# Optimization experiments

Hardware: AMD Instinct MI355X
Metric: run time of the kernel (lower is better)

The kernel has to match this reference:

```python
import jax, jax.numpy as jnp
import numpy as np

MODEL_BATCHES = 2048
NUM_POINTS = 8192
N_FUNCS = 8
REMOVE_ITERS = 51  # remove_points = 51 * model_batches -> first 51 iterations dropped


def setup_inputs() -> dict:
    key = jax.random.key(0)
    k1, k2, k3, k4, k5 = jax.random.split(key, 5)
    point = jax.random.normal(k1, (MODEL_BATCHES, 2, 1), dtype=jnp.float32) * 0.1
    optimized_weights = jax.random.normal(k2, (N_FUNCS, 2, 2), dtype=jnp.float32) * 0.5
    optimized_biases = jax.random.normal(k3, (N_FUNCS, 2, 1), dtype=jnp.float32) * 0.5
    optimized_function_ops = jax.random.uniform(k4, (N_FUNCS,), dtype=jnp.float32)
    index = jax.random.randint(k5, (MODEL_BATCHES, NUM_POINTS), 0, N_FUNCS, dtype=jnp.int32)
    return {
        "point": point,
        "optimized_weights": optimized_weights,
        "optimized_biases": optimized_biases,
        "optimized_function_ops": optimized_function_ops,
        "index": index,
    }


def reference(point, optimized_weights, optimized_biases, optimized_function_ops, index):
    mb = point.shape[0]

    def step(p, idx):  # p: [mb,2,1], idx: [mb]
        W = optimized_weights[idx]          # [mb,2,2]
        b = optimized_biases[idx]           # [mb,2,1]
        op = optimized_function_ops[idx]    # [mb]
        p_new = jnp.einsum('bij,bjk->bik', W, p) + b  # [mb,2,1]
        out = jnp.concatenate([p_new[:, :, 0], op[:, None]], axis=1)  # [mb,3]
        return p_new, out

    # scan over iterations: index.T is [num_points, mb]
    _, outs = jax.lax.scan(step, point, index.T)  # outs: [num_points, mb, 3]
    pts = outs.reshape(-1, 3)  # matches torch.cat along dim 0 then squeeze
    return pts[REMOVE_ITERS * mb:, :]
```

## Files before the change

kernel.cpp:

```cpp
#include <hip/hip_runtime.h>
#include <hip/hip_fp16.h>

#define MB   2048
#define NP   8192
#define NF   8
#define RM   51
#define NCH  128
#define CH   64
#define NW   16

typedef float        f32x4 __attribute__((ext_vector_type(4)));
typedef unsigned int u32;


__device__ __forceinline__ void build_tbl(u32 (*tbl)[4], const float* W,
                                          const float* B, const float* OPS, int tid)
{
    if (tid < NF) {
        const __half2 h0 = __floats2half2_rn(W[tid*4+0], W[tid*4+1]);
        const __half2 h1 = __floats2half2_rn(W[tid*4+2], W[tid*4+3]);
        const __half2 h2 = __floats2half2_rn(B[tid*2+0], B[tid*2+1]);
        const __half2 h3 = __floats2half2_rn(OPS ? OPS[tid] : 0.f, 0.f);
        tbl[tid][0] = __builtin_bit_cast(u32, h0);
        tbl[tid][1] = __builtin_bit_cast(u32, h1);
        tbl[tid][2] = __builtin_bit_cast(u32, h2);
        tbl[tid][3] = __builtin_bit_cast(u32, h3);
    }
}

__global__ __launch_bounds__(256, 4) void ifs_phase1(
    const int* __restrict__ idxg, const float* __restrict__ W,
    const float* __restrict__ B,
    float4* __restrict__ mapsA, float2* __restrict__ mapsC, u32* __restrict__ codes)
{
    __shared__ u32 ptile[256][NW + 1];
    __shared__ __align__(16) u32 tbl[NF][4];
    const int tid = threadIdx.x;
    build_tbl(tbl, W, B, nullptr, tid);

    const int c  = blockIdx.x >> 3;
    const int b0 = (blockIdx.x & 7) << 8;
    const int x8 = tid & 7, yy = tid >> 3;

    auto stage = [&](int seg) {
        #pragma unroll
        for (int p = 0; p < 8; ++p) {
            const int row = yy + p * 32;
            const int4 v = *(const int4*)(idxg + (size_t)(b0 + row) * NP
                                          + c * CH + seg * 32 + x8 * 4);
            ptile[row][seg * 8 + x8] =
                (u32)v.x | ((u32)v.y << 8) | ((u32)v.z << 16) | ((u32)v.w << 24);
        }
    };
    stage(0);
    __syncthreads();

    float a00 = 1.f, a01 = 0.f, a10 = 0.f, a11 = 1.f, c0 = 0.f, c1 = 0.f;
    for (int seg = 0; seg < 2; ++seg) {
        if (seg == 0) stage(1);
        #pragma unroll
        for (int j = 0; j < 8; ++j) {
            const u32 pc = ptile[tid][seg * 8 + j];
            #pragma unroll
            for (int e = 0; e < 4; ++e) {
                const int f = (pc >> (8 * e)) & 7;
                const uint4 u = *(const uint4*)&tbl[f][0];
                const float2 w0 = __half22float2(__builtin_bit_cast(__half2, u.x));
                const float2 w1 = __half22float2(__builtin_bit_cast(__half2, u.y));
                const float2 bb = __half22float2(__builtin_bit_cast(__half2, u.z));
                const float na00 = w0.x*a00 + w0.y*a10;
                const float na01 = w0.x*a01 + w0.y*a11;
                const float na10 = w1.x*a00 + w1.y*a10;
                const float na11 = w1.x*a01 + w1.y*a11;
                const float nc0  = w0.x*c0  + w0.y*c1 + bb.x;
                const float nc1  = w1.x*c0  + w1.y*c1 + bb.y;
                a00 = na00; a01 = na01; a10 = na10; a11 = na11; c0 = nc0; c1 = nc1;
            }
        }
        __syncthreads();
    }
    #pragma unroll
    for (int w = 0; w < NW; ++w)
        codes[((size_t)c * NW + w) * MB + b0 + tid] = ptile[tid][w];
    mapsA[(size_t)c * MB + b0 + tid] = make_float4(a00, a01, a10, a11);
    mapsC[(size_t)c * MB + b0 + tid] = make_float2(c0, c1);
}

__global__ __launch_bounds__(64) void ifs_phase2(
    const float2* __restrict__ point, const float4* __restrict__ mapsA,
    const float2* __restrict__ mapsC, float2* __restrict__ pe)
{
    const int b = blockIdx.x * 64 + threadIdx.x;
    float2 p = point[b];
    float4 A0[8], A1[8]; float2 C0[8], C1[8];
    #pragma unroll
    for (int k = 0; k < 8; ++k) {
        A0[k] = mapsA[(size_t)k * MB + b];
        C0[k] = mapsC[(size_t)k * MB + b];
    }
    for (int g = 0; g < 16; ++g) {
        if (g < 15) {
            #pragma unroll
            for (int k = 0; k < 8; ++k) {
                A1[k] = mapsA[(size_t)((g + 1) * 8 + k) * MB + b];
                C1[k] = mapsC[(size_t)((g + 1) * 8 + k) * MB + b];
            }
        }
        #pragma unroll
        for (int k = 0; k < 8; ++k) {
            pe[(size_t)(g * 8 + k) * MB + b] = p;
            const float nx = A0[k].x * p.x + A0[k].y * p.y + C0[k].x;
            const float ny = A0[k].z * p.x + A0[k].w * p.y + C0[k].y;
            p.x = nx; p.y = ny;
        }
        #pragma unroll
        for (int k = 0; k < 8; ++k) { A0[k] = A1[k]; C0[k] = C1[k]; }
    }
}

__global__ __launch_bounds__(256, 4) void ifs_phase3(
    const u32* __restrict__ codes, const float* __restrict__ W,
    const float* __restrict__ B, const float* __restrict__ OPS,
    const float2* __restrict__ pe, float* __restrict__ out)
{
    __shared__ __align__(16) float sbuf[2][4][256][3];
    __shared__ __align__(16) u32 tbl[NF][4];
    const int tid = threadIdx.x;
    build_tbl(tbl, W, B, OPS, tid);

    const int c  = blockIdx.x >> 3;
    const int b0 = (blockIdx.x & 7) << 8;
    const int b  = b0 + tid;

    u32 code[NW];
    #pragma unroll
    for (int w = 0; w < NW; ++w)
        code[w] = codes[((size_t)c * NW + w) * MB + b];
    const float2 p0 = pe[(size_t)c * MB + b];

    int s_[3];
    long long off[3];
    #pragma unroll
    for (int k = 0; k < 3; ++k) {
        const int w = 4 * (tid + 256 * k);
        s_[k] = w / 768;
        const int r = w - s_[k] * 768;
        off[k] = (long long)(c * CH + s_[k] - RM) * (MB * 3) + b0 * 3 + r;
    }
    const bool chk = (c == 0);
    float2 p = p0;
    __syncthreads();

    for (int g = 0; g < 16; ++g) {
        const int buf = g & 1;
        const u32 pc = code[g];
        #pragma unroll
        for (int s = 0; s < 4; ++s) {
            const int f = (pc >> (8 * s)) & 7;
            const uint4 u = *(const uint4*)&tbl[f][0];
            const float2 w0 = __half22float2(__builtin_bit_cast(__half2, u.x));
            const float2 w1 = __half22float2(__builtin_bit_cast(__half2, u.y));
            const float2 bb = __half22float2(__builtin_bit_cast(__half2, u.z));
            const float op  = __low2float(__builtin_bit_cast(__half2, u.w));
            const float nx = w0.x * p.x + w0.y * p.y + bb.x;
            const float ny = w1.x * p.x + w1.y * p.y + bb.y;
            p.x = nx; p.y = ny;
            sbuf[buf][s][tid][0] = nx;
            sbuf[buf][s][tid][1] = ny;
            sbuf[buf][s][tid][2] = op;
        }
        __syncthreads();
        const float* flat = &sbuf[buf][0][0][0];
        #pragma unroll
        for (int k = 0; k < 3; ++k) {
            if (!chk || (g * 4 + s_[k]) >= RM) {
                const f32x4 v = *(const f32x4*)(flat + 4 * (tid + 256 * k));
                __builtin_nontemporal_store(v, (f32x4*)(out + off[k]));
            }
            off[k] += 4LL * (MB * 3);
        }
    }
}

extern "C" void kernel_launch(void* const* d_in, const int* in_sizes, int n_in,
                              void* d_out, int out_size, void* d_ws, size_t ws_size,
                              hipStream_t stream) {
    const float* point = (const float*)d_in[0];
    const float* W     = (const float*)d_in[1];
    const float* B     = (const float*)d_in[2];
    const float* OPS   = (const float*)d_in[3];
    const int*   idx   = (const int*)  d_in[4];
    float*       out   = (float*)d_out;

    char* ws = (char*)d_ws;
    float4* mapsA = (float4*)(ws);
    float2* mapsC = (float2*)(ws + (size_t)NCH * MB * 16);
    float2* pe    = (float2*)(ws + (size_t)NCH * MB * 24);
    u32*    codes = (u32*)   (ws + (size_t)NCH * MB * 32);

    ifs_phase1<<<NCH * (MB / 256), 256, 0, stream>>>(idx, W, B, mapsA, mapsC, codes);
    ifs_phase2<<<MB / 64, 64, 0, stream>>>((const float2*)point, mapsA, mapsC, pe);
    ifs_phase3<<<NCH * (MB / 256), 256, 0, stream>>>(codes, W, B, OPS, pe, out);
}
```

Measured before the change: 76.48 us.

## Re-read index in phase 3 instead of writing packed codes; use fp32 tables

Phase 1 no longer writes the packed index codes to the workspace. Phase 3 instead re-reads the int32 index tile from global memory and packs it into 4-bit nibbles in a u16 shared tile. The fp16 lookup table is replaced with fp32 float4 tables, which removes the half-to-float conversions and restores full precision. The idea is to drop the codes write and read traffic, but phase 3 now reads the full int32 index array, about 64MB, a second time, so global traffic may go up.

```diff
diff --git a/kernel.cpp b/kernel.cpp
--- a/kernel.cpp
+++ b/kernel.cpp
@@ -1,5 +1,4 @@
 #include <hip/hip_runtime.h>
-#include <hip/hip_fp16.h>
 
 #define MB   2048
 #define NP   8192
@@ -7,81 +6,75 @@
 #define RM   51
 #define NCH  128
 #define CH   64
-#define NW   16
+#define COLS 17
 
-typedef float        f32x4 __attribute__((ext_vector_type(4)));
-typedef unsigned int u32;
+typedef float          f32x4 __attribute__((ext_vector_type(4)));
+typedef unsigned int   u32;
+typedef unsigned short u16;
+
+#define CMAP(g) ((((g) & 7) << 1) | ((g) >> 3))
 
 
-__device__ __forceinline__ void build_tbl(u32 (*tbl)[4], const float* W,
+__device__ __forceinline__ void build_tbl(float4* tA, float4* tB, const float* W,
                                           const float* B, const float* OPS, int tid)
 {
     if (tid < NF) {
-        const __half2 h0 = __floats2half2_rn(W[tid*4+0], W[tid*4+1]);
-        const __half2 h1 = __floats2half2_rn(W[tid*4+2], W[tid*4+3]);
-        const __half2 h2 = __floats2half2_rn(B[tid*2+0], B[tid*2+1]);
-        const __half2 h3 = __floats2half2_rn(OPS ? OPS[tid] : 0.f, 0.f);
-        tbl[tid][0] = __builtin_bit_cast(u32, h0);
-        tbl[tid][1] = __builtin_bit_cast(u32, h1);
-        tbl[tid][2] = __builtin_bit_cast(u32, h2);
-        tbl[tid][3] = __builtin_bit_cast(u32, h3);
+        tA[tid] = make_float4(W[tid*4+0], W[tid*4+1], W[tid*4+2], W[tid*4+3]);
+        tB[tid] = make_float4(B[tid*2+0], B[tid*2+1], OPS ? OPS[tid] : 0.f, 0.f);
+    }
+}
+
+__device__ __forceinline__ void stage_u16(
+    const int* __restrict__ idxg, u16 (*tile)[COLS],
+    int c, int b0, int x8, int yy, int seg)
+{
+    #pragma unroll
+    for (int p = 0; p < 8; ++p) {
+        const int row = yy + p * 32;
+        const int4 v = *(const int4*)(idxg + (size_t)(b0 + row) * NP
+                                      + c * CH + seg * 32 + x8 * 4);
+        tile[row][2 * x8 + seg] = (u16)(v.x | (v.y << 4) | (v.z << 8) | (v.w << 12));
     }
 }
 
 __global__ __launch_bounds__(256, 4) void ifs_phase1(
     const int* __restrict__ idxg, const float* __restrict__ W,
     const float* __restrict__ B,
-    float4* __restrict__ mapsA, float2* __restrict__ mapsC, u32* __restrict__ codes)
+    float4* __restrict__ mapsA, float2* __restrict__ mapsC)
 {
-    __shared__ u32 ptile[256][NW + 1];
-    __shared__ __align__(16) u32 tbl[NF][4];
+    __shared__ u16 tile[256][COLS];
+    __shared__ __align__(16) float4 tA[NF], tB[NF];
     const int tid = threadIdx.x;
-    build_tbl(tbl, W, B, nullptr, tid);
+    const int c   = blockIdx.x >> 3;
+    const int b0  = (blockIdx.x & 7) << 8;
+    const int x8  = tid & 7, yy = tid >> 3;
 
-    const int c  = blockIdx.x >> 3;
-    const int b0 = (blockIdx.x & 7) << 8;
-    const int x8 = tid & 7, yy = tid >> 3;
-
-    auto stage = [&](int seg) {
-        #pragma unroll
-        for (int p = 0; p < 8; ++p) {
-            const int row = yy + p * 32;
-            const int4 v = *(const int4*)(idxg + (size_t)(b0 + row) * NP
-                                          + c * CH + seg * 32 + x8 * 4);
-            ptile[row][seg * 8 + x8] =
-                (u32)v.x | ((u32)v.y << 8) | ((u32)v.z << 16) | ((u32)v.w << 24);
-        }
-    };
-    stage(0);
+    build_tbl(tA, tB, W, B, nullptr, tid);
+    stage_u16(idxg, tile, c, b0, x8, yy, 0);
     __syncthreads();
 
     float a00 = 1.f, a01 = 0.f, a10 = 0.f, a11 = 1.f, c0 = 0.f, c1 = 0.f;
     for (int seg = 0; seg < 2; ++seg) {
-        if (seg == 0) stage(1);
+        if (seg == 0) stage_u16(idxg, tile, c, b0, x8, yy, 1);
         #pragma unroll
         for (int j = 0; j < 8; ++j) {
-            const u32 pc = ptile[tid][seg * 8 + j];
+            const u32 pc = tile[tid][CMAP(seg * 8 + j)];
             #pragma unroll
             for (int e = 0; e < 4; ++e) {
-                const int f = (pc >> (8 * e)) & 7;
-                const uint4 u = *(const uint4*)&tbl[f][0];
-                const float2 w0 = __half22float2(__builtin_bit_cast(__half2, u.x));
-                const float2 w1 = __half22float2(__builtin_bit_cast(__half2, u.y));
-                const float2 bb = __half22float2(__builtin_bit_cast(__half2, u.z));
-                const float na00 = w0.x*a00 + w0.y*a10;
-                const float na01 = w0.x*a01 + w0.y*a11;
-                const float na10 = w1.x*a00 + w1.y*a10;
-                const float na11 = w1.x*a01 + w1.y*a11;
-                const float nc0  = w0.x*c0  + w0.y*c1 + bb.x;
-                const float nc1  = w1.x*c0  + w1.y*c1 + bb.y;
+                const int f = (pc >> (4 * e)) & 7;
+                const float4 w  = tA[f];
+                const float4 bb = tB[f];
+                const float na00 = w.x*a00 + w.y*a10;
+                const float na01 = w.x*a01 + w.y*a11;
+                const float na10 = w.z*a00 + w.w*a10;
+                const float na11 = w.z*a01 + w.w*a11;
+                const float nc0  = w.x*c0  + w.y*c1 + bb.x;
+                const float nc1  = w.z*c0  + w.w*c1 + bb.y;
                 a00 = na00; a01 = na01; a10 = na10; a11 = na11; c0 = nc0; c1 = nc1;
             }
         }
         __syncthreads();
     }
-    #pragma unroll
-    for (int w = 0; w < NW; ++w)
-        codes[((size_t)c * NW + w) * MB + b0 + tid] = ptile[tid][w];
     mapsA[(size_t)c * MB + b0 + tid] = make_float4(a00, a01, a10, a11);
     mapsC[(size_t)c * MB + b0 + tid] = make_float2(c0, c1);
 }
@@ -119,24 +112,23 @@
 }
 
 __global__ __launch_bounds__(256, 4) void ifs_phase3(
-    const u32* __restrict__ codes, const float* __restrict__ W,
+    const int* __restrict__ idxg, const float* __restrict__ W,
     const float* __restrict__ B, const float* __restrict__ OPS,
     const float2* __restrict__ pe, float* __restrict__ out)
 {
+    __shared__ u16 tile[256][COLS];
     __shared__ __align__(16) float sbuf[2][4][256][3];
-    __shared__ __align__(16) u32 tbl[NF][4];
+    __shared__ __align__(16) float4 tA[NF], tB[NF];
     const int tid = threadIdx.x;
-    build_tbl(tbl, W, B, OPS, tid);
+    const int c   = blockIdx.x >> 3;
+    const int b0  = (blockIdx.x & 7) << 8;
+    const int x8  = tid & 7, yy = tid >> 3;
 
-    const int c  = blockIdx.x >> 3;
-    const int b0 = (blockIdx.x & 7) << 8;
-    const int b  = b0 + tid;
+    build_tbl(tA, tB, W, B, OPS, tid);
+    stage_u16(idxg, tile, c, b0, x8, yy, 0);
+    stage_u16(idxg, tile, c, b0, x8, yy, 1);
 
-    u32 code[NW];
-    #pragma unroll
-    for (int w = 0; w < NW; ++w)
-        code[w] = codes[((size_t)c * NW + w) * MB + b];
-    const float2 p0 = pe[(size_t)c * MB + b];
+    float2 p = pe[(size_t)c * MB + b0 + tid];
 
     int s_[3];
     long long off[3];
@@ -148,26 +140,22 @@
         off[k] = (long long)(c * CH + s_[k] - RM) * (MB * 3) + b0 * 3 + r;
     }
     const bool chk = (c == 0);
-    float2 p = p0;
     __syncthreads();
 
     for (int g = 0; g < 16; ++g) {
         const int buf = g & 1;
-        const u32 pc = code[g];
+        const u32 pc = tile[tid][CMAP(g)];
         #pragma unroll
         for (int s = 0; s < 4; ++s) {
-            const int f = (pc >> (8 * s)) & 7;
-            const uint4 u = *(const uint4*)&tbl[f][0];
-            const float2 w0 = __half22float2(__builtin_bit_cast(__half2, u.x));
-            const float2 w1 = __half22float2(__builtin_bit_cast(__half2, u.y));
-            const float2 bb = __half22float2(__builtin_bit_cast(__half2, u.z));
-            const float op  = __low2float(__builtin_bit_cast(__half2, u.w));
-            const float nx = w0.x * p.x + w0.y * p.y + bb.x;
-            const float ny = w1.x * p.x + w1.y * p.y + bb.y;
+            const int f = (pc >> (4 * s)) & 7;
+            const float4 w  = tA[f];
+            const float4 bb = tB[f];
+            const float nx = w.x * p.x + w.y * p.y + bb.x;
+            const float ny = w.z * p.x + w.w * p.y + bb.y;
             p.x = nx; p.y = ny;
             sbuf[buf][s][tid][0] = nx;
             sbuf[buf][s][tid][1] = ny;
-            sbuf[buf][s][tid][2] = op;
+            sbuf[buf][s][tid][2] = bb.z;
         }
         __syncthreads();
         const float* flat = &sbuf[buf][0][0][0];
@@ -185,20 +173,19 @@
 extern "C" void kernel_launch(void* const* d_in, const int* in_sizes, int n_in,
                               void* d_out, int out_size, void* d_ws, size_t ws_size,
                               hipStream_t stream) {
-    const float* point = (const float*)d_in[0];
-    const float* W     = (const float*)d_in[1];
-    const float* B     = (const float*)d_in[2];
-    const float* OPS   = (const float*)d_in[3];
-    const int*   idx   = (const int*)  d_in[4];
-    float*       out   = (float*)d_out;
+    const float2* point = (const float2*)d_in[0];
+    const float*  W     = (const float*)d_in[1];
+    const float*  B     = (const float*)d_in[2];
+    const float*  OPS   = (const float*)d_in[3];
+    const int*    idx   = (const int*)  d_in[4];
+    float*        out   = (float*)d_out;
 
     char* ws = (char*)d_ws;
     float4* mapsA = (float4*)(ws);
     float2* mapsC = (float2*)(ws + (size_t)NCH * MB * 16);
     float2* pe    = (float2*)(ws + (size_t)NCH * MB * 24);
-    u32*    codes = (u32*)   (ws + (size_t)NCH * MB * 32);
 
-    ifs_phase1<<<NCH * (MB / 256), 256, 0, stream>>>(idx, W, B, mapsA, mapsC, codes);
-    ifs_phase2<<<MB / 64, 64, 0, stream>>>((const float2*)point, mapsA, mapsC, pe);
-    ifs_phase3<<<NCH * (MB / 256), 256, 0, stream>>>(codes, W, B, OPS, pe, out);
+    ifs_phase1<<<NCH * (MB / 256), 256, 0, stream>>>(idx, W, B, mapsA, mapsC);
+    ifs_phase2<<<MB / 64, 64, 0, stream>>>(point, mapsA, mapsC, pe);
+    ifs_phase3<<<NCH * (MB / 256), 256, 0, stream>>>(idx, W, B, OPS, pe, out);
 }
```

Result: slower. 86.05 us (+12.5%).
